# Optimization experiments

Hardware: AMD Instinct MI355X
Metric: run time of the kernel (lower is better)

## Reference

```python
import jax, jax.numpy as jnp
import numpy as np

E, C, K, S = 8, 128, 512, 512  # embedding_dim, channels, kernel_size, stride
NEG_SLOPE = 0.01  # torch F.leaky_relu default


def setup_inputs() -> dict:
    key = jax.random.key(0)
    ks = jax.random.split(key, 11)
    B, T = 4, 1_000_000
    sc = 0.05
    return {
        "x": jax.random.normal(ks[0], (B, T, E), jnp.float32),
        # ctx_conv: Conv1d(E, 2C, K, stride=S) -> weight (2C, E, K), bias (2C,)
        "ctx_conv_w": jax.random.normal(ks[1], (2 * C, E, K), jnp.float32) * sc,
        "ctx_conv_b": jax.random.normal(ks[2], (2 * C,), jnp.float32) * sc,
        # ctx_share: Conv1d(C, C, 1) -> (C, C) pointwise
        "ctx_share_w": jax.random.normal(ks[3], (C, C), jnp.float32) * sc,
        "ctx_share_b": jax.random.normal(ks[4], (C,), jnp.float32) * sc,
        "main_conv_w": jax.random.normal(ks[5], (2 * C, E, K), jnp.float32) * sc,
        "main_conv_b": jax.random.normal(ks[6], (2 * C,), jnp.float32) * sc,
        "main_share_w": jax.random.normal(ks[7], (C, C), jnp.float32) * sc,
        "main_share_b": jax.random.normal(ks[8], (C,), jnp.float32) * sc,
        # gct_proj: Linear(C, C) -> weight (C, C) (y = g @ W.T + b)
        "gct_proj_w": jax.random.normal(ks[9], (C, C), jnp.float32) * sc,
        "gct_proj_b": jax.random.normal(ks[10], (C,), jnp.float32) * sc,
    }


def _leaky(x):
    return jnp.where(x >= 0, x, NEG_SLOPE * x)


def _glu(x):  # GLU over channel dim 1
    a, b = jnp.split(x, 2, axis=1)
    return a * jax.nn.sigmoid(b)


def _conv(z, w, b):
    # z: (B, Cin, T), w: (Cout, Cin, K) -> (B, Cout, T_out), stride S, VALID
    y = jax.lax.conv_general_dilated(z, w, (S,), 'VALID',
                                     dimension_numbers=('NCH', 'OIH', 'NCH'))
    return y + b[None, :, None]


def _branch_act(z, wc, bc, ws, bs):
    # glu(conv(z)) -> leaky_relu(1x1 share conv)
    h = _glu(_conv(z, wc, bc))                                   # (B, C, T_out)
    h = _leaky(jnp.einsum('oc,bct->bot', ws, h) + bs[None, :, None])
    return h


def reference(x, ctx_conv_w, ctx_conv_b, ctx_share_w, ctx_share_b,
              main_conv_w, main_conv_b, main_share_w, main_share_b,
              gct_proj_w, gct_proj_b):
    z = jnp.transpose(x, (0, 2, 1))  # (B, E, T)
    # Context branch: global max over time of ctx activations (GCG context).
    g = _branch_act(z, ctx_conv_w, ctx_conv_b, ctx_share_w, ctx_share_b)
    gct = jnp.max(g, axis=-1)  # (B, C)
    # Main branch with global channel gating.
    h = _branch_act(z, main_conv_w, main_conv_b, main_share_w, main_share_b)  # (B, C, T_out)
    q = jnp.tanh(gct @ gct_proj_w.T + gct_proj_b)                # (B, C)
    gate = jax.nn.sigmoid(jnp.einsum('bct,bc->bt', h, q))        # (B, T_out)
    out = jnp.max(h * gate[:, None, :], axis=-1)                 # (B, C)
    return out
```

## Files before the change

kernel.cpp:

```cpp
#include <hip/hip_runtime.h>
#include <hip/hip_bf16.h>
#include <cmath>

#define B_    4
#define T_    1000000
#define E_    8
#define C_    128
#define NCH   512
#define KK    4096
#define TOUT  1953
#define TP    1956
#define TPAD  2048
#define NT2   31

typedef __attribute__((ext_vector_type(8))) short bf16x8;
typedef __attribute__((ext_vector_type(4))) float f32x4;

__device__ __forceinline__ float sigmoidf_(float v) { return 1.f / (1.f + __expf(-v)); }

__global__ __launch_bounds__(256) void prep_inputs(
    const float* __restrict__ x,
    const float* __restrict__ wc, const float* __restrict__ bc,
    const float* __restrict__ wm, const float* __restrict__ bm,
    __hip_bfloat16* __restrict__ xb2, __hip_bfloat16* __restrict__ Wn2,
    float* __restrict__ bias_t) {
  __shared__ float row[KK];
  const int bid = blockIdx.x;
  if (bid < NCH) {
    const int n = bid, br = n >> 8, o = n & 255;
    const float* wsrc = (br ? wm : wc) + (size_t)o * KK;
    for (int i = threadIdx.x; i < KK; i += 256) row[i] = wsrc[i];
    __syncthreads();
    const int nt = n >> 4, nr = n & 15;
    for (int k = threadIdx.x; k < KK; k += 256) {
      int kpos = k >> 3, e = k & 7;
      size_t addr = (((size_t)nt * 128 + (k >> 5)) * 64
                     + (size_t)((k >> 3) & 3) * 16 + nr) * 8 + (k & 7);
      Wn2[addr] = __float2bfloat16(row[e * 512 + kpos]);
    }
    if (threadIdx.x == 0) bias_t[n] = (br ? bm : bc)[o];
  } else {
    size_t gid = (size_t)(bid - NCH) * 256 + threadIdx.x;
    size_t idx8 = gid * 8;
    size_t b = idx8 >> 23, rem = idx8 & ((1ull << 23) - 1);
    int lane = (int)((rem >> 3) & 63);
    int kc   = (int)((rem >> 9) & 127);
    int tt   = (int)(rem >> 16);
    int t = tt * 16 + (lane & 15);
    int k = kc * 32 + (lane >> 4) * 8;
    union { __hip_bfloat16 h[8]; uint4 u; } o;
    if (t < TOUT) {
      const float* src = x + b * 8000000ull + (size_t)t * KK + k;
      float4 f0 = *(const float4*)(src);
      float4 f1 = *(const float4*)(src + 4);
      o.h[0] = __float2bfloat16(f0.x); o.h[1] = __float2bfloat16(f0.y);
      o.h[2] = __float2bfloat16(f0.z); o.h[3] = __float2bfloat16(f0.w);
      o.h[4] = __float2bfloat16(f1.x); o.h[5] = __float2bfloat16(f1.y);
      o.h[6] = __float2bfloat16(f1.z); o.h[7] = __float2bfloat16(f1.w);
    } else {
      o.u = make_uint4(0, 0, 0, 0);
    }
    *(uint4*)(xb2 + idx8) = o.u;
  }
}

__global__ __launch_bounds__(512, 2) void mfma_gemm(
    const __hip_bfloat16* __restrict__ xb2, const __hip_bfloat16* __restrict__ Wn2,
    float* __restrict__ u2) {
  const int tid  = threadIdx.x;
  const int lane = tid & 63, wave = tid >> 6;
  const int wt = wave & 3, wn = wave >> 2;

  const int L   = blockIdx.x;
  const int xcd = L & 7;
  const int r   = L >> 3;
  const int nb  = r & 3;
  const int sh  = r >> 2;
  const int s   = sh * 8 + xcd;
  const int tblk = s & 15, b = s >> 4;
  const int t0 = tblk * 128, n0 = nb * 128;

  const size_t FR = 512;
  const __hip_bfloat16* aB = xb2
      + ((size_t)(b * 128 + (t0 >> 4) + wt * 2) * 128) * FR + (size_t)lane * 8;
  const __hip_bfloat16* bB = Wn2
      + ((size_t)((n0 >> 4) + wn * 4) * 128) * FR + (size_t)lane * 8;

  f32x4 acc[2][4];
#pragma unroll
  for (int i = 0; i < 2; ++i)
#pragma unroll
    for (int j = 0; j < 4; ++j) acc[i][j] = (f32x4)(0.0f);

  bf16x8 A0[2][2], B0[4][2], A1[2][2], B1[4][2];

  auto load_set = [&](bf16x8 (&aF)[2][2], bf16x8 (&bF)[4][2], int kc) {
#pragma unroll
    for (int i = 0; i < 2; ++i)
#pragma unroll
      for (int c = 0; c < 2; ++c)
        aF[i][c] = *(const bf16x8*)(aB + (size_t)(i * 128 + kc + c) * FR);
#pragma unroll
    for (int j = 0; j < 4; ++j)
#pragma unroll
      for (int c = 0; c < 2; ++c)
        bF[j][c] = *(const bf16x8*)(bB + (size_t)(j * 128 + kc + c) * FR);
  };
  auto do_mfma = [&](bf16x8 (&aF)[2][2], bf16x8 (&bF)[4][2]) {
#pragma unroll
    for (int c = 0; c < 2; ++c)
#pragma unroll
      for (int i = 0; i < 2; ++i)
#pragma unroll
        for (int j = 0; j < 4; ++j)
          acc[i][j] = __builtin_amdgcn_mfma_f32_16x16x32_bf16(aF[i][c], bF[j][c],
                                                              acc[i][j], 0, 0, 0);
  };

  load_set(A0, B0, 0);
  for (int kc = 0; kc < 128; kc += 4) {
    load_set(A1, B1, kc + 2);
    do_mfma(A0, B0);
    if (kc + 4 < 128) load_set(A0, B0, kc + 4);
    do_mfma(A1, B1);
  }

  const int crow = (lane >> 4) * 4;
  const int ccol = lane & 15;
#pragma unroll
  for (int j = 0; j < 4; ++j) {
    int n = n0 + wn * 64 + j * 16 + ccol;
    float* urow = u2 + ((size_t)n * B_ + b) * TP;
#pragma unroll
    for (int i = 0; i < 2; ++i) {
      int t = t0 + wt * 32 + i * 16 + crow;
      if (t < TOUT) *(f32x4*)(urow + t) = acc[i][j];
    }
  }
}

__global__ __launch_bounds__(256) void share_act(
    const float* __restrict__ u2, const float* __restrict__ bias_t,
    const float* __restrict__ wsc, const float* __restrict__ bsc,
    const float* __restrict__ wsm, const float* __restrict__ bsm,
    float* __restrict__ hmain, float* __restrict__ gct_part) {
  __shared__ float Wl[128 * 132];
  __shared__ float ul[128 * 68];
  const int tid  = threadIdx.x;
  const int tile = blockIdx.x;
  const int b    = blockIdx.y;
  const int br   = blockIdx.z;
  const int t0   = tile * 64;
  const float* ws = br ? wsm : wsc;
  const float* bs = br ? bsm : bsc;

  for (int g = tid; g < 16384; g += 256) {
    int co = g >> 7, cp = g & 127;
    Wl[cp * 132 + co] = ws[g];
  }
  const size_t base_v = ((size_t)(br * 256) * B_ + b) * TP;
  const size_t base_g = ((size_t)(br * 256 + 128) * B_ + b) * TP;
  for (int g = tid; g < 8192; g += 256) {
    int cp = g >> 6, t = g & 63;
    float v = 0.f;
    if (t0 + t < TOUT) {
      float va = u2[base_v + (size_t)cp * B_ * TP + t0 + t] + bias_t[br * 256 + cp];
      float vg = u2[base_g + (size_t)cp * B_ * TP + t0 + t] + bias_t[br * 256 + 128 + cp];
      v = va * sigmoidf_(vg);
    }
    ul[cp * 68 + t] = v;
  }
  __syncthreads();

  const int ty = tid >> 4, tx = tid & 15;
  float acc[8][4];
#pragma unroll
  for (int i = 0; i < 8; ++i)
#pragma unroll
    for (int j = 0; j < 4; ++j) acc[i][j] = 0.f;

  for (int cp = 0; cp < 128; ++cp) {
    float4 a0 = *(const float4*)&Wl[cp*132 + ty*4];
    float4 a1 = *(const float4*)&Wl[cp*132 + 64 + ty*4];
    float4 b4 = *(const float4*)&ul[cp*68 + tx*4];
    float av[8] = {a0.x,a0.y,a0.z,a0.w,a1.x,a1.y,a1.z,a1.w};
    float bv[4] = {b4.x,b4.y,b4.z,b4.w};
#pragma unroll
    for (int i = 0; i < 8; ++i)
#pragma unroll
      for (int j = 0; j < 4; ++j) acc[i][j] = fmaf(av[i], bv[j], acc[i][j]);
  }

  float mloc[8];
#pragma unroll
  for (int i = 0; i < 8; ++i) mloc[i] = -INFINITY;
#pragma unroll
  for (int i = 0; i < 8; ++i) {
    int c = (i < 4) ? (ty*4 + i) : (64 + ty*4 + (i - 4));
    float bias = bs[c];
#pragma unroll
    for (int j = 0; j < 4; ++j) {
      int t = t0 + tx*4 + j;
      if (t >= TOUT) continue;
      float v = acc[i][j] + bias;
      v = (v >= 0.f) ? v : 0.01f * v;
      if (br == 1) {
        hmain[((size_t)b * 128 + c) * TOUT + t] = v;
      } else {
        mloc[i] = fmaxf(mloc[i], v);
      }
    }
  }
  if (br == 0) {
    __syncthreads();
    float* red = ul;
#pragma unroll
    for (int i = 0; i < 8; ++i) {
      int c = (i < 4) ? (ty*4 + i) : (64 + ty*4 + (i - 4));
      red[c * 16 + tx] = mloc[i];
    }
    __syncthreads();
    if (tid < 128) {
      float m = -INFINITY;
#pragma unroll
      for (int k = 0; k < 16; ++k) m = fmaxf(m, red[tid * 16 + k]);
      gct_part[((size_t)b * 128 + tid) * NT2 + tile] = m;
    }
  }
}

__global__ void gct_q(const float* __restrict__ gct_part, const float* __restrict__ wp,
                      const float* __restrict__ bp, float* __restrict__ q) {
  int b = blockIdx.x, tid = threadIdx.x;
  __shared__ float g[128];
  float m = -INFINITY;
  for (int tl = 0; tl < NT2; ++tl) m = fmaxf(m, gct_part[((size_t)b * 128 + tid) * NT2 + tl]);
  g[tid] = m;
  __syncthreads();
  float s = bp[tid];
  for (int c = 0; c < 128; ++c) s = fmaf(g[c], wp[tid * 128 + c], s);
  q[b * 128 + tid] = tanhf(s);
}

__global__ __launch_bounds__(256) void gate_max(
    const float* __restrict__ hmain, const float* __restrict__ q,
    float* __restrict__ out_part) {
  __shared__ float hl[128 * 68];
  __shared__ float ql[128];
  __shared__ float red[256];
  __shared__ float gl[64];
  int tid = threadIdx.x, tile = blockIdx.x, b = blockIdx.y;
  int t0 = tile * 64;
  for (int g = tid; g < 8192; g += 256) {
    int c = g >> 6, t = g & 63;
    hl[c * 68 + t] = (t0 + t < TOUT) ? hmain[((size_t)b * 128 + c) * TOUT + t0 + t] : 0.f;
  }
  if (tid < 128) ql[tid] = q[b * 128 + tid];
  __syncthreads();
  {
    int t = tid & 63, cy = tid >> 6;
    float s = 0.f;
#pragma unroll
    for (int cc = 0; cc < 32; ++cc) s = fmaf(hl[(cy * 32 + cc) * 68 + t], ql[cy * 32 + cc], s);
    red[cy * 64 + t] = s;
  }
  __syncthreads();
  if (tid < 64) {
    float s = red[tid] + red[64 + tid] + red[128 + tid] + red[192 + tid];
    gl[tid] = sigmoidf_(s);
  }
  __syncthreads();
  {
    int c = tid >> 1, th = tid & 1;
    float m = -INFINITY;
#pragma unroll
    for (int tt = 0; tt < 32; ++tt) {
      int t = th * 32 + tt;
      if (t0 + t < TOUT) m = fmaxf(m, hl[c * 68 + t] * gl[t]);
    }
    red[c * 2 + th] = m;
  }
  __syncthreads();
  if (tid < 128) out_part[((size_t)b * 128 + tid) * NT2 + tile] = fmaxf(red[tid * 2], red[tid * 2 + 1]);
}

__global__ void final_max(const float* __restrict__ out_part, float* __restrict__ out) {
  int idx = blockIdx.x * 256 + threadIdx.x;
  if (idx < 512) {
    float m = -INFINITY;
    for (int tl = 0; tl < NT2; ++tl) m = fmaxf(m, out_part[(size_t)idx * NT2 + tl]);
    out[idx] = m;
  }
}

extern "C" void kernel_launch(void* const* d_in, const int* in_sizes, int n_in,
                              void* d_out, int out_size, void* d_ws, size_t ws_size,
                              hipStream_t stream) {
  const float* x      = (const float*)d_in[0];
  const float* ctx_w  = (const float*)d_in[1];
  const float* ctx_b  = (const float*)d_in[2];
  const float* ctx_sw = (const float*)d_in[3];
  const float* ctx_sb = (const float*)d_in[4];
  const float* main_w = (const float*)d_in[5];
  const float* main_b = (const float*)d_in[6];
  const float* main_sw= (const float*)d_in[7];
  const float* main_sb= (const float*)d_in[8];
  const float* gp_w   = (const float*)d_in[9];
  const float* gp_b   = (const float*)d_in[10];

  char* w = (char*)d_ws;
  __hip_bfloat16* xb2 = (__hip_bfloat16*)(w);
  __hip_bfloat16* Wn2 = (__hip_bfloat16*)(w + 67108864);
  float* bias_t  = (float*)(w + 71303168);
  float* u2      = (float*)(w + 71305216);
  float* hmain   = (float*)(w + 87328768);
  float* gct_part= (float*)(w + 91328512);
  float* q       = (float*)(w + 91392000);
  float* out_part= (float*)(w + 91394048);

  prep_inputs<<<NCH + 16384, 256, 0, stream>>>(x, ctx_w, ctx_b, main_w, main_b,
                                               xb2, Wn2, bias_t);
  mfma_gemm<<<256, 512, 0, stream>>>(xb2, Wn2, u2);
  share_act<<<dim3(NT2, B_, 2), 256, 0, stream>>>(u2, bias_t, ctx_sw, ctx_sb,
                                                  main_sw, main_sb, hmain, gct_part);
  gct_q<<<B_, 128, 0, stream>>>(gct_part, gp_w, gp_b, q);
  gate_max<<<dim3(NT2, B_), 256, 0, stream>>>(hmain, q, out_part);
  final_max<<<2, 256, 0, stream>>>(out_part, (float*)d_out);
}
```

Measured before the change: 315.8 us.

## Fuse main share conv with gating and max, and retile MFMA GEMM

The main-branch 1x1 share conv, the gct projection with tanh, the gate dot product with sigmoid, and the gated max are merged into one kernel. This removes the hmain intermediate write and read-back plus two kernel launches. The context branch gets its own specialized kernel. The MFMA GEMM is retiled to 64-wide time blocks with a 2x2 accumulator per wave, doubling the grid to 512 blocks for more parallelism at the cost of less register-level reuse per wave.

Result: slower. 344.1 us (+8.9%).

```diff
diff --git a/kernel.cpp b/kernel.cpp
--- a/kernel.cpp
+++ b/kernel.cpp
@@ -10,7 +10,6 @@
 #define KK    4096
 #define TOUT  1953
 #define TP    1956
-#define TPAD  2048
 #define NT2   31
 
 typedef __attribute__((ext_vector_type(8))) short bf16x8;
@@ -69,50 +68,49 @@
     float* __restrict__ u2) {
   const int tid  = threadIdx.x;
   const int lane = tid & 63, wave = tid >> 6;
-  const int wt = wave & 3, wn = wave >> 2;
+  const int wt = wave & 1, wn = wave >> 1;
 
   const int L   = blockIdx.x;
   const int xcd = L & 7;
-  const int r   = L >> 3;
-  const int nb  = r & 3;
-  const int sh  = r >> 2;
-  const int s   = sh * 8 + xcd;
-  const int tblk = s & 15, b = s >> 4;
-  const int t0 = tblk * 128, n0 = nb * 128;
+  const int nb  = (L >> 3) & 3;
+  const int g   = L >> 5;
+  const int s   = g * 8 + xcd;
+  const int tblk = s & 31, b = s >> 5;
+  const int t0 = tblk * 64, n0 = nb * 128;
 
   const size_t FR = 512;
   const __hip_bfloat16* aB = xb2
-      + ((size_t)(b * 128 + (t0 >> 4) + wt * 2) * 128) * FR + (size_t)lane * 8;
+      + ((size_t)(b * 128 + tblk * 4 + wt * 2) * 128) * FR + (size_t)lane * 8;
   const __hip_bfloat16* bB = Wn2
-      + ((size_t)((n0 >> 4) + wn * 4) * 128) * FR + (size_t)lane * 8;
-
-  f32x4 acc[2][4];
+      + ((size_t)(nb * 8 + wn * 2) * 128) * FR + (size_t)lane * 8;
+
+  f32x4 acc[2][2];
 #pragma unroll
   for (int i = 0; i < 2; ++i)
 #pragma unroll
-    for (int j = 0; j < 4; ++j) acc[i][j] = (f32x4)(0.0f);
-
-  bf16x8 A0[2][2], B0[4][2], A1[2][2], B1[4][2];
-
-  auto load_set = [&](bf16x8 (&aF)[2][2], bf16x8 (&bF)[4][2], int kc) {
+    for (int j = 0; j < 2; ++j) acc[i][j] = (f32x4)(0.0f);
+
+  bf16x8 A0[2][2], B0[2][2], A1[2][2], B1[2][2];
+
+  auto load_set = [&](bf16x8 (&aF)[2][2], bf16x8 (&bF)[2][2], int kc) {
 #pragma unroll
     for (int i = 0; i < 2; ++i)
 #pragma unroll
       for (int c = 0; c < 2; ++c)
         aF[i][c] = *(const bf16x8*)(aB + (size_t)(i * 128 + kc + c) * FR);
 #pragma unroll
-    for (int j = 0; j < 4; ++j)
+    for (int j = 0; j < 2; ++j)
 #pragma unroll
       for (int c = 0; c < 2; ++c)
         bF[j][c] = *(const bf16x8*)(bB + (size_t)(j * 128 + kc + c) * FR);
   };
-  auto do_mfma = [&](bf16x8 (&aF)[2][2], bf16x8 (&bF)[4][2]) {
+  auto do_mfma = [&](bf16x8 (&aF)[2][2], bf16x8 (&bF)[2][2]) {
 #pragma unroll
     for (int c = 0; c < 2; ++c)
 #pragma unroll
       for (int i = 0; i < 2; ++i)
 #pragma unroll
-        for (int j = 0; j < 4; ++j)
+        for (int j = 0; j < 2; ++j)
           acc[i][j] = __builtin_amdgcn_mfma_f32_16x16x32_bf16(aF[i][c], bF[j][c],
                                                               acc[i][j], 0, 0, 0);
   };
@@ -128,8 +126,8 @@
   const int crow = (lane >> 4) * 4;
   const int ccol = lane & 15;
 #pragma unroll
-  for (int j = 0; j < 4; ++j) {
-    int n = n0 + wn * 64 + j * 16 + ccol;
+  for (int j = 0; j < 2; ++j) {
+    int n = n0 + wn * 32 + j * 16 + ccol;
     float* urow = u2 + ((size_t)n * B_ + b) * TP;
 #pragma unroll
     for (int i = 0; i < 2; ++i) {
@@ -139,33 +137,29 @@
   }
 }
 
-__global__ __launch_bounds__(256) void share_act(
+__global__ __launch_bounds__(256) void share_ctx(
     const float* __restrict__ u2, const float* __restrict__ bias_t,
     const float* __restrict__ wsc, const float* __restrict__ bsc,
-    const float* __restrict__ wsm, const float* __restrict__ bsm,
-    float* __restrict__ hmain, float* __restrict__ gct_part) {
+    float* __restrict__ gct_part) {
   __shared__ float Wl[128 * 132];
   __shared__ float ul[128 * 68];
   const int tid  = threadIdx.x;
   const int tile = blockIdx.x;
   const int b    = blockIdx.y;
-  const int br   = blockIdx.z;
   const int t0   = tile * 64;
-  const float* ws = br ? wsm : wsc;
-  const float* bs = br ? bsm : bsc;
 
   for (int g = tid; g < 16384; g += 256) {
     int co = g >> 7, cp = g & 127;
-    Wl[cp * 132 + co] = ws[g];
-  }
-  const size_t base_v = ((size_t)(br * 256) * B_ + b) * TP;
-  const size_t base_g = ((size_t)(br * 256 + 128) * B_ + b) * TP;
+    Wl[cp * 132 + co] = wsc[g];
+  }
+  const size_t base_v = (size_t)b * TP;
+  const size_t base_g = ((size_t)128 * B_ + b) * TP;
   for (int g = tid; g < 8192; g += 256) {
     int cp = g >> 6, t = g & 63;
     float v = 0.f;
     if (t0 + t < TOUT) {
-      float va = u2[base_v + (size_t)cp * B_ * TP + t0 + t] + bias_t[br * 256 + cp];
-      float vg = u2[base_g + (size_t)cp * B_ * TP + t0 + t] + bias_t[br * 256 + 128 + cp];
+      float va = u2[base_v + (size_t)cp * B_ * TP + t0 + t] + bias_t[cp];
+      float vg = u2[base_g + (size_t)cp * B_ * TP + t0 + t] + bias_t[128 + cp];
       v = va * sigmoidf_(vg);
     }
     ul[cp * 68 + t] = v;
@@ -197,91 +191,143 @@
 #pragma unroll
   for (int i = 0; i < 8; ++i) {
     int c = (i < 4) ? (ty*4 + i) : (64 + ty*4 + (i - 4));
-    float bias = bs[c];
+    float bias = bsc[c];
 #pragma unroll
     for (int j = 0; j < 4; ++j) {
       int t = t0 + tx*4 + j;
       if (t >= TOUT) continue;
       float v = acc[i][j] + bias;
-      v = (v >= 0.f) ? v : 0.01f * v;
-      if (br == 1) {
-        hmain[((size_t)b * 128 + c) * TOUT + t] = v;
-      } else {
-        mloc[i] = fmaxf(mloc[i], v);
-      }
-    }
-  }
-  if (br == 0) {
-    __syncthreads();
-    float* red = ul;
+      mloc[i] = fmaxf(mloc[i], (v >= 0.f) ? v : 0.01f * v);
+    }
+  }
+  __syncthreads();
+#pragma unroll
+  for (int i = 0; i < 8; ++i) {
+    int c = (i < 4) ? (ty*4 + i) : (64 + ty*4 + (i - 4));
+    ul[c * 16 + tx] = mloc[i];
+  }
+  __syncthreads();
+  if (tid < 128) {
+    float m = -INFINITY;
+#pragma unroll
+    for (int k = 0; k < 16; ++k) m = fmaxf(m, ul[tid * 16 + k]);
+    gct_part[((size_t)b * 128 + tid) * NT2 + tile] = m;
+  }
+}
+
+__global__ __launch_bounds__(256) void share_main_gate(
+    const float* __restrict__ u2, const float* __restrict__ bias_t,
+    const float* __restrict__ wsm, const float* __restrict__ bsm,
+    const float* __restrict__ gct_part,
+    const float* __restrict__ wp, const float* __restrict__ bp,
+    float* __restrict__ out_part) {
+  __shared__ float Wl[128 * 132];
+  __shared__ float ul[128 * 68];
+  __shared__ float gbuf[128];
+  __shared__ float ql[128];
+  const int tid  = threadIdx.x;
+  const int tile = blockIdx.x;
+  const int b    = blockIdx.y;
+  const int t0   = tile * 64;
+
+  for (int g = tid; g < 16384; g += 256) {
+    int co = g >> 7, cp = g & 127;
+    Wl[cp * 132 + co] = wsm[g];
+  }
+  const size_t base_v = ((size_t)256 * B_ + b) * TP;
+  const size_t base_g = ((size_t)384 * B_ + b) * TP;
+  for (int g = tid; g < 8192; g += 256) {
+    int cp = g >> 6, t = g & 63;
+    float v = 0.f;
+    if (t0 + t < TOUT) {
+      float va = u2[base_v + (size_t)cp * B_ * TP + t0 + t] + bias_t[256 + cp];
+      float vg = u2[base_g + (size_t)cp * B_ * TP + t0 + t] + bias_t[384 + cp];
+      v = va * sigmoidf_(vg);
+    }
+    ul[cp * 68 + t] = v;
+  }
+  if (tid < 128) {
+    float m = -INFINITY;
+    for (int tl = 0; tl < NT2; ++tl)
+      m = fmaxf(m, gct_part[((size_t)b * 128 + tid) * NT2 + tl]);
+    gbuf[tid] = m;
+  }
+  __syncthreads();
+  if (tid < 128) {
+    float sq = bp[tid];
+    for (int c = 0; c < 128; ++c) sq = fmaf(gbuf[c], wp[tid * 128 + c], sq);
+    ql[tid] = tanhf(sq);
+  }
+
+  const int ty = tid >> 4, tx = tid & 15;
+  float acc[8][4];
+#pragma unroll
+  for (int i = 0; i < 8; ++i)
+#pragma unroll
+    for (int j = 0; j < 4; ++j) acc[i][j] = 0.f;
+
+  for (int cp = 0; cp < 128; ++cp) {
+    float4 a0 = *(const float4*)&Wl[cp*132 + ty*4];
+    float4 a1 = *(const float4*)&Wl[cp*132 + 64 + ty*4];
+    float4 b4 = *(const float4*)&ul[cp*68 + tx*4];
+    float av[8] = {a0.x,a0.y,a0.z,a0.w,a1.x,a1.y,a1.z,a1.w};
+    float bv[4] = {b4.x,b4.y,b4.z,b4.w};
+#pragma unroll
+    for (int i = 0; i < 8; ++i)
+#pragma unroll
+      for (int j = 0; j < 4; ++j) acc[i][j] = fmaf(av[i], bv[j], acc[i][j]);
+  }
+
+  float h[8][4];
+#pragma unroll
+  for (int i = 0; i < 8; ++i) {
+    int c = (i < 4) ? (ty*4 + i) : (64 + ty*4 + (i - 4));
+    float bias = bsm[c];
+#pragma unroll
+    for (int j = 0; j < 4; ++j) {
+      float v = acc[i][j] + bias;
+      h[i][j] = (v >= 0.f) ? v : 0.01f * v;
+    }
+  }
+  __syncthreads();
+
+#pragma unroll
+  for (int j = 0; j < 4; ++j) {
+    float pg = 0.f;
 #pragma unroll
     for (int i = 0; i < 8; ++i) {
       int c = (i < 4) ? (ty*4 + i) : (64 + ty*4 + (i - 4));
-      red[c * 16 + tx] = mloc[i];
-    }
-    __syncthreads();
-    if (tid < 128) {
-      float m = -INFINITY;
-#pragma unroll
-      for (int k = 0; k < 16; ++k) m = fmaxf(m, red[tid * 16 + k]);
-      gct_part[((size_t)b * 128 + tid) * NT2 + tile] = m;
-    }
-  }
-}
-
-__global__ void gct_q(const float* __restrict__ gct_part, const float* __restrict__ wp,
-                      const float* __restrict__ bp, float* __restrict__ q) {
-  int b = blockIdx.x, tid = threadIdx.x;
-  __shared__ float g[128];
-  float m = -INFINITY;
-  for (int tl = 0; tl < NT2; ++tl) m = fmaxf(m, gct_part[((size_t)b * 128 + tid) * NT2 + tl]);
-  g[tid] = m;
-  __syncthreads();
-  float s = bp[tid];
-  for (int c = 0; c < 128; ++c) s = fmaf(g[c], wp[tid * 128 + c], s);
-  q[b * 128 + tid] = tanhf(s);
-}
-
-__global__ __launch_bounds__(256) void gate_max(
-    const float* __restrict__ hmain, const float* __restrict__ q,
-    float* __restrict__ out_part) {
-  __shared__ float hl[128 * 68];
-  __shared__ float ql[128];
-  __shared__ float red[256];
-  __shared__ float gl[64];
-  int tid = threadIdx.x, tile = blockIdx.x, b = blockIdx.y;
-  int t0 = tile * 64;
-  for (int g = tid; g < 8192; g += 256) {
-    int c = g >> 6, t = g & 63;
-    hl[c * 68 + t] = (t0 + t < TOUT) ? hmain[((size_t)b * 128 + c) * TOUT + t0 + t] : 0.f;
-  }
-  if (tid < 128) ql[tid] = q[b * 128 + tid];
-  __syncthreads();
-  {
-    int t = tid & 63, cy = tid >> 6;
-    float s = 0.f;
-#pragma unroll
-    for (int cc = 0; cc < 32; ++cc) s = fmaf(hl[(cy * 32 + cc) * 68 + t], ql[cy * 32 + cc], s);
-    red[cy * 64 + t] = s;
+      pg = fmaf(h[i][j], ql[c], pg);
+    }
+    ul[(tx*4 + j) * 16 + ty] = pg;
   }
   __syncthreads();
   if (tid < 64) {
-    float s = red[tid] + red[64 + tid] + red[128 + tid] + red[192 + tid];
-    gl[tid] = sigmoidf_(s);
-  }
-  __syncthreads();
-  {
-    int c = tid >> 1, th = tid & 1;
-    float m = -INFINITY;
-#pragma unroll
-    for (int tt = 0; tt < 32; ++tt) {
-      int t = th * 32 + tt;
-      if (t0 + t < TOUT) m = fmaxf(m, hl[c * 68 + t] * gl[t]);
-    }
-    red[c * 2 + th] = m;
-  }
-  __syncthreads();
-  if (tid < 128) out_part[((size_t)b * 128 + tid) * NT2 + tile] = fmaxf(red[tid * 2], red[tid * 2 + 1]);
+    float sg = 0.f;
+#pragma unroll
+    for (int y = 0; y < 16; ++y) sg += ul[tid * 16 + y];
+    ul[1024 + tid] = sigmoidf_(sg);
+  }
+  __syncthreads();
+
+#pragma unroll
+  for (int i = 0; i < 8; ++i) {
+    int c = (i < 4) ? (ty*4 + i) : (64 + ty*4 + (i - 4));
+    float m = -INFINITY;
+#pragma unroll
+    for (int j = 0; j < 4; ++j) {
+      int t = t0 + tx*4 + j;
+      if (t < TOUT) m = fmaxf(m, h[i][j] * ul[1024 + tx*4 + j]);
+    }
+    ul[2048 + c * 16 + tx] = m;
+  }
+  __syncthreads();
+  if (tid < 128) {
+    float m = -INFINITY;
+#pragma unroll
+    for (int k = 0; k < 16; ++k) m = fmaxf(m, ul[2048 + tid * 16 + k]);
+    out_part[((size_t)b * 128 + tid) * NT2 + tile] = m;
+  }
 }
 
 __global__ void final_max(const float* __restrict__ out_part, float* __restrict__ out) {
@@ -313,17 +359,14 @@
   __hip_bfloat16* Wn2 = (__hip_bfloat16*)(w + 67108864);
   float* bias_t  = (float*)(w + 71303168);
   float* u2      = (float*)(w + 71305216);
-  float* hmain   = (float*)(w + 87328768);
-  float* gct_part= (float*)(w + 91328512);
-  float* q       = (float*)(w + 91392000);
-  float* out_part= (float*)(w + 91394048);
+  float* gct_part= (float*)(w + 87328768);
+  float* out_part= (float*)(w + 87392256);
 
   prep_inputs<<<NCH + 16384, 256, 0, stream>>>(x, ctx_w, ctx_b, main_w, main_b,
                                                xb2, Wn2, bias_t);
-  mfma_gemm<<<256, 512, 0, stream>>>(xb2, Wn2, u2);
-  share_act<<<dim3(NT2, B_, 2), 256, 0, stream>>>(u2, bias_t, ctx_sw, ctx_sb,
-                                                  main_sw, main_sb, hmain, gct_part);
-  gct_q<<<B_, 128, 0, stream>>>(gct_part, gp_w, gp_b, q);
-  gate_max<<<dim3(NT2, B_), 256, 0, stream>>>(hmain, q, out_part);
+  mfma_gemm<<<512, 512, 0, stream>>>(xb2, Wn2, u2);
+  share_ctx<<<dim3(NT2, B_), 256, 0, stream>>>(u2, bias_t, ctx_sw, ctx_sb, gct_part);
+  share_main_gate<<<dim3(NT2, B_), 256, 0, stream>>>(u2, bias_t, main_sw, main_sb,
+                                                     gct_part, gp_w, gp_b, out_part);
   final_max<<<2, 256, 0, stream>>>(out_part, (float*)d_out);
 }
```
